# Kernel tuning notes

Hardware: AMD Instinct MI355X
Metric: run time of the kernel (lower is better)

## Reference

```python
import jax, jax.numpy as jnp
import numpy as np

B, N, IN_DIM = 2, 512, 512
MEM, HID = 300, 64
NEG_SLOPE = 0.01


def setup_inputs() -> dict:
    key = jax.random.key(0)
    ks = jax.random.split(key, 10)
    feature = jax.random.normal(ks[0], (B, N, IN_DIM), dtype=jnp.float32)
    adj = jax.random.randint(ks[1], (B, N, N), 0, 2).astype(jnp.float32)
    s = 0.05
    # per-layer node projections W[l]
    w0 = jax.random.normal(ks[2], (IN_DIM, MEM), dtype=jnp.float32) * s
    b0 = jnp.zeros((MEM,), dtype=jnp.float32)
    w1 = jax.random.normal(ks[3], (MEM, MEM), dtype=jnp.float32) * s
    b1 = jnp.zeros((MEM,), dtype=jnp.float32)
    # shared attention MLP (afcs): Linear(2*MEM, HID) -> ReLU -> Linear(HID, 1)
    a1_w = jax.random.normal(ks[4], (2 * MEM, HID), dtype=jnp.float32) * s
    a1_b = jnp.zeros((HID,), dtype=jnp.float32)
    a2_w = jax.random.normal(ks[5], (HID, 1), dtype=jnp.float32) * s
    a2_b = jnp.zeros((1,), dtype=jnp.float32)
    return {"feature": feature, "adj": adj, "w0": w0, "b0": b0, "w1": w1,
            "b1": b1, "a1_w": a1_w, "a1_b": a1_b, "a2_w": a2_w, "a2_b": a2_b}


def _gat_layer(h_in, adj, w, b, a1_w, a1_b, a2_w, a2_b):
    h = h_in @ w + b                                   # (B,N,M)
    # cat([h_i, h_j]) @ a1_w split into the two halves (same math, no N^2*2M tensor)
    s_i = h @ a1_w[:MEM]                               # (B,N,H)
    s_j = h @ a1_w[MEM:]                               # (B,N,H)
    z = jax.nn.relu(s_i[:, :, None, :] + s_j[:, None, :, :] + a1_b)   # (B,N,N,H)
    e = (z @ a2_w)[..., 0] + a2_b[0]                   # (B,N,N)
    e = jax.nn.leaky_relu(e, negative_slope=NEG_SLOPE)
    b_, n_ = adj.shape[0], adj.shape[1]
    dmask = adj.reshape(b_, n_ * n_)
    logits = e.reshape(b_, n_ * n_) * dmask + (1.0 - dmask) * (-1e30)
    # NOTE: softmax over ALL N*N flattened edges (faithful to original dim=1)
    att = jax.nn.softmax(logits, axis=1).reshape(b_, n_, n_)
    return jnp.einsum('bij,bjd->bid', att, h)


def reference(feature, adj, w0, b0, w1, b1, a1_w, a1_b, a2_w, a2_b):
    f = _gat_layer(feature, adj, w0, b0, a1_w, a1_b, a2_w, a2_b)
    f = _gat_layer(f, adj, w1, b1, a1_w, a1_b, a2_w, a2_b)  # dropout = identity (eval)
    return f
```

## Files before the change

### kernel.cpp

```cpp
#include <hip/hip_runtime.h>

namespace {

constexpr int B_  = 2;
constexpr int N_  = 512;
constexpr int IN_ = 512;
constexpr int M_  = 300;
constexpr int H_  = 64;
constexpr float SLOPE_ = 0.01f;

constexpr long OFF_CW1AI = 0;
constexpr long OFF_CW1AJ = OFF_CW1AI + 19200;
constexpr long OFF_BS1I  = OFF_CW1AJ + 19200;
constexpr long OFF_BS1J  = OFF_BS1I  + 64;
constexpr long OFF_H0S   = OFF_BS1J  + 64;
constexpr long OFF_SI0S  = OFF_H0S   + 3L * 307200;
constexpr long OFF_SJ0S  = OFF_SI0S  + 4L * 65536;
constexpr long OFF_F1S   = OFF_SJ0S  + 4L * 65536;
constexpr long OFF_H1S   = OFF_F1S   + 3L * 307200;
constexpr long OFF_SI1S  = OFF_H1S   + 2L * 307200;
constexpr long OFF_SJ1S  = OFF_SI1S  + 2L * 65536;
constexpr long OFF_ZP0   = OFF_SJ1S  + 2L * 65536;
constexpr long OFF_ZP1   = OFF_ZP0   + 512;
constexpr long OFF_P0    = OFF_ZP1   + 512;
constexpr long OFF_P1    = OFF_P0    + 524288;

__device__ __forceinline__ float4 f4add(float4 a, float4 b) {
    a.x += b.x; a.y += b.y; a.z += b.z; a.w += b.w; return a;
}

struct JobsK {
    const float* A[5]; long afs[5];
    const float* W[5]; long wfs[5];
    const float* bias[5]; const float* Zp[5];
    float* C[5]; long cslice[5];
    int K[5]; int lda[5]; int Cc[5]; int R[5]; int split[5];
    int off[5]; int njobs;
};

template<int TPB, int AFOLD, int WFOLD>
__global__ __launch_bounds__(TPB)
void gemm_jobs(JobsK jb)
{
    constexpr int TM  = (TPB == 256) ? 64 : 32;
    constexpr int TN  = TM;
    constexpr int APT = 32 * TM / TPB;
    constexpr int AQW = 32 / APT;
    constexpr int WQW = TPB / 32;
    constexpr int WPT = TN / WQW;
    constexpr int TCW = TN / 4;

    __shared__ __align__(16) float As[32][TM + 4];
    __shared__ __align__(16) float Ws[32][TN + 4];
    __shared__ float zred[4];

    const int bid = blockIdx.x;
    int j = jb.njobs - 1;
    while (j > 0 && bid < jb.off[j]) --j;
    const int local = bid - jb.off[j];

    const float* __restrict__ A = jb.A[j];  const long afs = jb.afs[j];
    const float* __restrict__ W = jb.W[j];  const long wfs = jb.wfs[j];
    const float* bias = jb.bias[j];
    const float* Zp   = jb.Zp[j];
    float* __restrict__ C = jb.C[j];
    const int K = jb.K[j], lda = jb.lda[j], Cc = jb.Cc[j], R = jb.R[j];
    const int split = jb.split[j];

    const int tx  = (Cc + TN - 1) / TN;
    const int ty  = (R + TM - 1) / TM;
    const int nrc = tx * ty;
    const int tile  = local % nrc;
    const int slice = local / nrc;
    const int row0 = (tile / tx) * TM;
    const int col0 = (tile % tx) * TN;
    const int nslab = (K + 31) >> 5;
    const int spl   = (nslab + split - 1) / split;
    const int kb    = slice * spl * 32;
    const int Ke    = min(K, kb + spl * 32);
    C += (long)slice * jb.cslice[j];

    const int t  = threadIdx.x;
    const int ar = t / AQW, aq = t % AQW;
    const int arow = min(row0 + ar, R - 1);
    const int wr = t / WQW, wq = t % WQW;
    const int tr = t / TCW, tc = t % TCW;

    float4 av[APT / 4], wv[WPT / 4];

    auto loadA = [&](int k0) {
        #pragma unroll
        for (int f = 0; f < APT / 4; ++f) {
            const int k = k0 + aq * APT + f * 4;
            const long base = (long)arow * lda + k;
            float4 r = make_float4(0.f, 0.f, 0.f, 0.f);
            if (k + 3 < Ke) {
                #pragma unroll
                for (int s = 0; s < AFOLD; ++s)
                    r = f4add(r, *(const float4*)(A + (long)s * afs + base));
            } else {
                #pragma unroll
                for (int u = 0; u < 4; ++u)
                    if (k + u < Ke) {
                        float v = 0.f;
                        #pragma unroll
                        for (int s = 0; s < AFOLD; ++s)
                            v += A[(long)s * afs + base + u];
                        (&r.x)[u] = v;
                    }
            }
            av[f] = r;
        }
    };
    auto loadW = [&](int k0) {
        const int gk = k0 + wr;
        #pragma unroll
        for (int f = 0; f < WPT / 4; ++f) {
            const int c = col0 + wq * WPT + f * 4;
            float4 r = make_float4(0.f, 0.f, 0.f, 0.f);
            if (gk < Ke) {
                const long base = (long)gk * Cc + c;
                if (c + 3 < Cc) {
                    #pragma unroll
                    for (int s = 0; s < WFOLD; ++s)
                        r = f4add(r, *(const float4*)(W + (long)s * wfs + base));
                } else {
                    #pragma unroll
                    for (int u = 0; u < 4; ++u)
                        if (c + u < Cc) {
                            float v = 0.f;
                            #pragma unroll
                            for (int s = 0; s < WFOLD; ++s)
                                v += W[(long)s * wfs + base + u];
                            (&r.x)[u] = v;
                        }
                }
            }
            wv[f] = r;
        }
    };

    float acc[4][4] = {};
    loadA(kb);
    loadW(kb);

    for (int k0 = kb; k0 < Ke; k0 += 32) {
        #pragma unroll
        for (int f = 0; f < APT / 4; ++f) {
            #pragma unroll
            for (int c = 0; c < 4; ++c) {
                const int kk = aq * APT + f * 4 + c;
                const int s  = (kk >> 3) & 3;
                As[kk][ar ^ (s << 2)] = (&av[f].x)[c];
            }
        }
        #pragma unroll
        for (int f = 0; f < WPT / 4; ++f)
            *(float4*)&Ws[wr][wq * WPT + 4 * f] = wv[f];
        __syncthreads();

        if (k0 + 32 < Ke) {
            loadA(k0 + 32);
            loadW(k0 + 32);
        }

        #pragma unroll
        for (int k = 0; k < 32; ++k) {
            const int s = (k >> 3) & 3;
            const float4 a4 = *(const float4*)&As[k][(tr ^ s) * 4];
            const float4 w4 = *(const float4*)&Ws[k][tc * 4];
            const float a_[4] = {a4.x, a4.y, a4.z, a4.w};
            #pragma unroll
            for (int i = 0; i < 4; ++i) {
                acc[i][0] = fmaf(a_[i], w4.x, acc[i][0]);
                acc[i][1] = fmaf(a_[i], w4.y, acc[i][1]);
                acc[i][2] = fmaf(a_[i], w4.z, acc[i][2]);
                acc[i][3] = fmaf(a_[i], w4.w, acc[i][3]);
            }
        }
        __syncthreads();
    }

    float scale = 1.0f;
    if (Zp != nullptr) {
        if constexpr (TPB == 256) {
            float v = Zp[t];
            #pragma unroll
            for (int off = 32; off > 0; off >>= 1)
                v += __shfl_down(v, off, 64);
            if ((t & 63) == 0) zred[t >> 6] = v;
            __syncthreads();
            scale = 1.0f / (zred[0] + zred[1] + zred[2] + zred[3]);
        } else {
            float v = Zp[t] + Zp[t + 64] + Zp[t + 128] + Zp[t + 192];
            #pragma unroll
            for (int off = 32; off > 0; off >>= 1)
                v += __shfl_down(v, off, 64);
            scale = 1.0f / __shfl(v, 0, 64);
        }
    }

    const int cbase = col0 + tc * 4;
    float bv[4] = {0.f, 0.f, 0.f, 0.f};
    if (bias != nullptr && slice == 0) {
        #pragma unroll
        for (int u = 0; u < 4; ++u)
            if (cbase + u < Cc) bv[u] = bias[cbase + u];
    }
    #pragma unroll
    for (int i = 0; i < 4; ++i) {
        const int r = row0 + tr * 4 + i;
        if (r < R) {
            if (cbase + 3 < Cc) {
                float4 o;
                o.x = fmaf(acc[i][0], scale, bv[0]);
                o.y = fmaf(acc[i][1], scale, bv[1]);
                o.z = fmaf(acc[i][2], scale, bv[2]);
                o.w = fmaf(acc[i][3], scale, bv[3]);
                *(float4*)(C + (long)r * Cc + cbase) = o;
            } else {
                #pragma unroll
                for (int u = 0; u < 4; ++u)
                    if (cbase + u < Cc)
                        C[(long)r * Cc + cbase + u] = fmaf(acc[i][u], scale, bv[u]);
            }
        }
    }
}

template<int FOLD>
__global__ __launch_bounds__(256)
void attn_k(const float* __restrict__ si, const float* __restrict__ sj,
            const float* __restrict__ adj, const float* __restrict__ a2w,
            const float* __restrict__ a2b, float* __restrict__ p,
            float* __restrict__ Zpart)
{
    __shared__ __align__(16) float Si[32][68];
    __shared__ __align__(16) float Sj[32][68];
    __shared__ float red[4];

    const int g    = blockIdx.x;
    const int b    = g >> 8;
    const int tile = g & 255;
    const int i0 = (tile >> 4) * 32;
    const int j0 = (tile & 15) * 32;
    const int t  = threadIdx.x;

    {
        const int r  = t >> 3;
        const int hc = (t & 7) * 8;
        const long gib = ((long)(b * N_ + i0 + r)) * H_ + hc;
        const long gjb = ((long)(b * N_ + j0 + r)) * H_ + hc;
        float4 a0 = make_float4(0.f, 0.f, 0.f, 0.f);
        float4 a1 = a0, b0v = a0, b1v = a0;
        #pragma unroll
        for (int s = 0; s < FOLD; ++s) {
            const float* gi = si + (long)s * 65536 + gib;
            const float* gj = sj + (long)s * 65536 + gjb;
            a0  = f4add(a0,  *(const float4*)(gi));
            a1  = f4add(a1,  *(const float4*)(gi + 4));
            b0v = f4add(b0v, *(const float4*)(gj));
            b1v = f4add(b1v, *(const float4*)(gj + 4));
        }
        *(float4*)&Si[r][hc]     = a0;
        *(float4*)&Si[r][hc + 4] = a1;
        *(float4*)&Sj[r][hc]     = b0v;
        *(float4*)&Sj[r][hc + 4] = b1v;
    }
    __syncthreads();

    const int i  = t >> 3;
    const int jl = t & 7;

    float e[4] = {0.f, 0.f, 0.f, 0.f};
    #pragma unroll
    for (int h0 = 0; h0 < H_; h0 += 4) {
        const float4 a4 = *(const float4*)&Si[i][h0];
        const float w0v = a2w[h0 + 0];
        const float w1v = a2w[h0 + 1];
        const float w2v = a2w[h0 + 2];
        const float w3v = a2w[h0 + 3];
        #pragma unroll
        for (int u = 0; u < 4; ++u) {
            const float4 b4 = *(const float4*)&Sj[jl + 8 * u][h0];
            e[u] = fmaf(fmaxf(a4.x + b4.x, 0.f), w0v, e[u]);
            e[u] = fmaf(fmaxf(a4.y + b4.y, 0.f), w1v, e[u]);
            e[u] = fmaf(fmaxf(a4.z + b4.z, 0.f), w2v, e[u]);
            e[u] = fmaf(fmaxf(a4.w + b4.w, 0.f), w3v, e[u]);
        }
    }

    const float a2bv = a2b[0];
    const long rowbase = ((long)(b * N_ + i0 + i)) * N_ + j0 + jl;
    float lsum = 0.f;
    #pragma unroll
    for (int u = 0; u < 4; ++u) {
        float ev = e[u] + a2bv;
        ev = (ev >= 0.f) ? ev : SLOPE_ * ev;
        const float m  = adj[rowbase + 8 * u];
        const float pv = m * __expf(ev);
        p[rowbase + 8 * u] = pv;
        lsum += pv;
    }

    #pragma unroll
    for (int off = 32; off > 0; off >>= 1)
        lsum += __shfl_down(lsum, off, 64);
    if ((t & 63) == 0) red[t >> 6] = lsum;
    __syncthreads();
    if (t == 0)
        Zpart[b * 256 + tile] = red[0] + red[1] + red[2] + red[3];
}

}

extern "C" void kernel_launch(void* const* d_in, const int* in_sizes, int n_in,
                              void* d_out, int out_size, void* d_ws, size_t ws_size,
                              hipStream_t stream)
{
    (void)in_sizes; (void)n_in; (void)out_size; (void)ws_size;
    const float* feature = (const float*)d_in[0];
    const float* adj     = (const float*)d_in[1];
    const float* w0      = (const float*)d_in[2];
    const float* b0      = (const float*)d_in[3];
    const float* w1      = (const float*)d_in[4];
    const float* b1      = (const float*)d_in[5];
    const float* a1w     = (const float*)d_in[6];
    const float* a1b     = (const float*)d_in[7];
    const float* a2w     = (const float*)d_in[8];
    const float* a2b     = (const float*)d_in[9];
    float* out = (float*)d_out;
    float* ws  = (float*)d_ws;

    float* cW1Ai = ws + OFF_CW1AI;
    float* cW1Aj = ws + OFF_CW1AJ;
    float* bs1i  = ws + OFF_BS1I;
    float* bs1j  = ws + OFF_BS1J;
    float* h0s   = ws + OFF_H0S;
    float* si0s  = ws + OFF_SI0S;
    float* sj0s  = ws + OFF_SJ0S;
    float* f1s   = ws + OFF_F1S;
    float* h1s   = ws + OFF_H1S;
    float* si1s  = ws + OFF_SI1S;
    float* sj1s  = ws + OFF_SJ1S;
    float* Zp0   = ws + OFF_ZP0;
    float* Zp1   = ws + OFF_ZP1;
    float* p0    = ws + OFF_P0;
    float* p1    = ws + OFF_P1;

    const float* Ai = a1w;
    const float* Aj = a1w + (long)M_ * H_;

    auto set_job = [](JobsK& jb, int j, const float* A, long afs,
                      const float* W, long wfs, const float* bias,
                      const float* Zp, float* C, long cslice,
                      int K, int lda, int Cc, int R, int split,
                      int TM, int& tiles) {
        jb.A[j] = A; jb.afs[j] = afs;
        jb.W[j] = W; jb.wfs[j] = wfs;
        jb.bias[j] = bias; jb.Zp[j] = Zp;
        jb.C[j] = C; jb.cslice[j] = cslice;
        jb.K[j] = K; jb.lda[j] = lda; jb.Cc[j] = Cc; jb.R[j] = R;
        jb.split[j] = split;
        jb.off[j] = tiles;
        tiles += ((R + TM - 1) / TM) * ((Cc + TM - 1) / TM) * split;
    };

    {
        JobsK jb; int tiles = 0;
        set_job(jb, 0, feature, 0, w0, 0, b0, nullptr, h0s, 307200,
                IN_, IN_, M_, 1024, 3, 64, tiles);
        set_job(jb, 1, w1, 0, Ai, 0, nullptr, nullptr, cW1Ai, 0,
                M_, M_, H_, M_, 1, 64, tiles);
        set_job(jb, 2, w1, 0, Aj, 0, nullptr, nullptr, cW1Aj, 0,
                M_, M_, H_, M_, 1, 64, tiles);
        set_job(jb, 3, b1, 0, Ai, 0, nullptr, nullptr, bs1i, 0,
                M_, M_, H_, 1, 1, 64, tiles);
        set_job(jb, 4, b1, 0, Aj, 0, a1b, nullptr, bs1j, 0,
                M_, M_, H_, 1, 1, 64, tiles);
        jb.njobs = 5;
        gemm_jobs<256, 1, 1><<<dim3(tiles), dim3(256), 0, stream>>>(jb);
    }

    {
        JobsK jb; int tiles = 0;
        set_job(jb, 0, h0s, 307200, Ai, 0, nullptr, nullptr, si0s, 65536,
                M_, M_, H_, 1024, 4, 64, tiles);
        set_job(jb, 1, h0s, 307200, Aj, 0, a1b, nullptr, sj0s, 65536,
                M_, M_, H_, 1024, 4, 64, tiles);
        jb.njobs = 2;
        gemm_jobs<256, 3, 1><<<dim3(tiles), dim3(256), 0, stream>>>(jb);
    }

    attn_k<4><<<dim3(512), dim3(256), 0, stream>>>(
        si0s, sj0s, adj, a2w, a2b, p0, Zp0);

    {
        JobsK jb; int tiles = 0;
        set_job(jb, 0, p0, 0, h0s, 307200, nullptr, Zp0, f1s, 307200,
                N_, N_, M_, N_, 3, 64, tiles);
        set_job(jb, 1, p0 + 262144, 0, h0s + 153600, 307200, nullptr,
                Zp0 + 256, f1s + 153600, 307200,
                N_, N_, M_, N_, 3, 64, tiles);
        jb.njobs = 2;
        gemm_jobs<256, 1, 3><<<dim3(tiles), dim3(256), 0, stream>>>(jb);
    }

    {
        JobsK jb; int tiles = 0;
        set_job(jb, 0, f1s, 307200, w1, 0, b1, nullptr, h1s, 307200,
                M_, M_, M_, 1024, 2, 64, tiles);
        set_job(jb, 1, f1s, 307200, cW1Ai, 0, bs1i, nullptr, si1s, 65536,
                M_, M_, H_, 1024, 2, 64, tiles);
        set_job(jb, 2, f1s, 307200, cW1Aj, 0, bs1j, nullptr, sj1s, 65536,
                M_, M_, H_, 1024, 2, 64, tiles);
        jb.njobs = 3;
        gemm_jobs<256, 3, 1><<<dim3(tiles), dim3(256), 0, stream>>>(jb);
    }

    attn_k<2><<<dim3(512), dim3(256), 0, stream>>>(
        si1s, sj1s, adj, a2w, a2b, p1, Zp1);

    {
        JobsK jb; int tiles = 0;
        set_job(jb, 0, p1, 0, h1s, 307200, nullptr, Zp1, out, 0,
                N_, N_, M_, N_, 1, 32, tiles);
        set_job(jb, 1, p1 + 262144, 0, h1s + 153600, 307200, nullptr,
                Zp1 + 256, out + 153600, 0,
                N_, N_, M_, N_, 1, 32, tiles);
        jb.njobs = 2;
        gemm_jobs<64, 1, 2><<<dim3(tiles), dim3(64), 0, stream>>>(jb);
    }
}
```

Measured before the change: 211.1 us.

## Fuse s_i/s_j projections into attention kernel and drop split-K partial buffers

Each attention block now computes its 32-row slices of s_i and s_j from h directly, so the separate s_i/s_j GEMM launches and their slice-sum buffers are gone. Split-K with partial-sum folding is removed from every GEMM, and the layer-1 h1 projection runs as extra blocks inside the second attention launch. This cuts the launch count from seven to five and removes intermediate global traffic. The cost is redundant projection work: every attention block recomputes s_i/s_j over K=300, roughly 16 times over, and the non-split GEMMs have fewer blocks, which lowers parallelism.

```diff
diff --git a/kernel.cpp b/kernel.cpp
--- a/kernel.cpp
+++ b/kernel.cpp
@@ -2,112 +2,55 @@
 
 namespace {
 
-constexpr int B_  = 2;
-constexpr int N_  = 512;
-constexpr int IN_ = 512;
-constexpr int M_  = 300;
-constexpr int H_  = 64;
+constexpr int N_ = 512;
+constexpr int M_ = 300;
+constexpr int H_ = 64;
 constexpr float SLOPE_ = 0.01f;
 
 constexpr long OFF_CW1AI = 0;
 constexpr long OFF_CW1AJ = OFF_CW1AI + 19200;
 constexpr long OFF_BS1I  = OFF_CW1AJ + 19200;
 constexpr long OFF_BS1J  = OFF_BS1I  + 64;
-constexpr long OFF_H0S   = OFF_BS1J  + 64;
-constexpr long OFF_SI0S  = OFF_H0S   + 3L * 307200;
-constexpr long OFF_SJ0S  = OFF_SI0S  + 4L * 65536;
-constexpr long OFF_F1S   = OFF_SJ0S  + 4L * 65536;
-constexpr long OFF_H1S   = OFF_F1S   + 3L * 307200;
-constexpr long OFF_SI1S  = OFF_H1S   + 2L * 307200;
-constexpr long OFF_SJ1S  = OFF_SI1S  + 2L * 65536;
-constexpr long OFF_ZP0   = OFF_SJ1S  + 2L * 65536;
+constexpr long OFF_H0    = OFF_BS1J  + 64;
+constexpr long OFF_F1    = OFF_H0    + 307200;
+constexpr long OFF_H1    = OFF_F1    + 307200;
+constexpr long OFF_ZP0   = OFF_H1    + 307200;
 constexpr long OFF_ZP1   = OFF_ZP0   + 512;
 constexpr long OFF_P0    = OFF_ZP1   + 512;
 constexpr long OFF_P1    = OFF_P0    + 524288;
 
-__device__ __forceinline__ float4 f4add(float4 a, float4 b) {
-    a.x += b.x; a.y += b.y; a.z += b.z; a.w += b.w; return a;
-}
-
-struct JobsK {
-    const float* A[5]; long afs[5];
-    const float* W[5]; long wfs[5];
-    const float* bias[5]; const float* Zp[5];
-    float* C[5]; long cslice[5];
-    int K[5]; int lda[5]; int Cc[5]; int R[5]; int split[5];
-    int off[5]; int njobs;
-};
-
-template<int TPB, int AFOLD, int WFOLD>
-__global__ __launch_bounds__(TPB)
-void gemm_jobs(JobsK jb)
+__device__ __forceinline__ void gemm_tile64(
+    const float* __restrict__ A, const float* __restrict__ W,
+    const float* __restrict__ bias, const float* __restrict__ Zp,
+    float* __restrict__ C, int K, int lda, int Cc, int R, int local,
+    float* smem)
 {
-    constexpr int TM  = (TPB == 256) ? 64 : 32;
-    constexpr int TN  = TM;
-    constexpr int APT = 32 * TM / TPB;
-    constexpr int AQW = 32 / APT;
-    constexpr int WQW = TPB / 32;
-    constexpr int WPT = TN / WQW;
-    constexpr int TCW = TN / 4;
-
-    __shared__ __align__(16) float As[32][TM + 4];
-    __shared__ __align__(16) float Ws[32][TN + 4];
-    __shared__ float zred[4];
-
-    const int bid = blockIdx.x;
-    int j = jb.njobs - 1;
-    while (j > 0 && bid < jb.off[j]) --j;
-    const int local = bid - jb.off[j];
-
-    const float* __restrict__ A = jb.A[j];  const long afs = jb.afs[j];
-    const float* __restrict__ W = jb.W[j];  const long wfs = jb.wfs[j];
-    const float* bias = jb.bias[j];
-    const float* Zp   = jb.Zp[j];
-    float* __restrict__ C = jb.C[j];
-    const int K = jb.K[j], lda = jb.lda[j], Cc = jb.Cc[j], R = jb.R[j];
-    const int split = jb.split[j];
-
-    const int tx  = (Cc + TN - 1) / TN;
-    const int ty  = (R + TM - 1) / TM;
-    const int nrc = tx * ty;
-    const int tile  = local % nrc;
-    const int slice = local / nrc;
-    const int row0 = (tile / tx) * TM;
-    const int col0 = (tile % tx) * TN;
-    const int nslab = (K + 31) >> 5;
-    const int spl   = (nslab + split - 1) / split;
-    const int kb    = slice * spl * 32;
-    const int Ke    = min(K, kb + spl * 32);
-    C += (long)slice * jb.cslice[j];
+    float (*As)[68] = (float(*)[68])smem;
+    float (*Ws)[68] = (float(*)[68])(smem + 2176);
+    float* zred = smem + 4352;
+
+    const int tx   = (Cc + 63) >> 6;
+    const int row0 = (local / tx) * 64;
+    const int col0 = (local % tx) * 64;
 
     const int t  = threadIdx.x;
-    const int ar = t / AQW, aq = t % AQW;
+    const int ar = t >> 2, aq = t & 3;
     const int arow = min(row0 + ar, R - 1);
-    const int wr = t / WQW, wq = t % WQW;
-    const int tr = t / TCW, tc = t % TCW;
-
-    float4 av[APT / 4], wv[WPT / 4];
-
+    const int wr = t >> 3, wq = t & 7;
+    const int tr = t >> 4, tc = t & 15;
+
+    float4 av[2], wv[2];
     auto loadA = [&](int k0) {
         #pragma unroll
-        for (int f = 0; f < APT / 4; ++f) {
-            const int k = k0 + aq * APT + f * 4;
-            const long base = (long)arow * lda + k;
+        for (int f = 0; f < 2; ++f) {
+            const int k = k0 + aq * 8 + f * 4;
             float4 r = make_float4(0.f, 0.f, 0.f, 0.f);
-            if (k + 3 < Ke) {
-                #pragma unroll
-                for (int s = 0; s < AFOLD; ++s)
-                    r = f4add(r, *(const float4*)(A + (long)s * afs + base));
+            if (k + 3 < K) {
+                r = *(const float4*)(A + (long)arow * lda + k);
             } else {
                 #pragma unroll
                 for (int u = 0; u < 4; ++u)
-                    if (k + u < Ke) {
-                        float v = 0.f;
-                        #pragma unroll
-                        for (int s = 0; s < AFOLD; ++s)
-                            v += A[(long)s * afs + base + u];
-                        (&r.x)[u] = v;
-                    }
+                    if (k + u < K) (&r.x)[u] = A[(long)arow * lda + k + u];
             }
             av[f] = r;
         }
@@ -115,25 +58,16 @@
     auto loadW = [&](int k0) {
         const int gk = k0 + wr;
         #pragma unroll
-        for (int f = 0; f < WPT / 4; ++f) {
-            const int c = col0 + wq * WPT + f * 4;
+        for (int f = 0; f < 2; ++f) {
+            const int c = col0 + wq * 8 + f * 4;
             float4 r = make_float4(0.f, 0.f, 0.f, 0.f);
-            if (gk < Ke) {
-                const long base = (long)gk * Cc + c;
+            if (gk < K) {
                 if (c + 3 < Cc) {
-                    #pragma unroll
-                    for (int s = 0; s < WFOLD; ++s)
-                        r = f4add(r, *(const float4*)(W + (long)s * wfs + base));
+                    r = *(const float4*)(W + (long)gk * Cc + c);
                 } else {
                     #pragma unroll
                     for (int u = 0; u < 4; ++u)
-                        if (c + u < Cc) {
-                            float v = 0.f;
-                            #pragma unroll
-                            for (int s = 0; s < WFOLD; ++s)
-                                v += W[(long)s * wfs + base + u];
-                            (&r.x)[u] = v;
-                        }
+                        if (c + u < Cc) (&r.x)[u] = W[(long)gk * Cc + c + u];
                 }
             }
             wv[f] = r;
@@ -141,28 +75,24 @@
     };
 
     float acc[4][4] = {};
-    loadA(kb);
-    loadW(kb);
-
-    for (int k0 = kb; k0 < Ke; k0 += 32) {
-        #pragma unroll
-        for (int f = 0; f < APT / 4; ++f) {
+    loadA(0);
+    loadW(0);
+
+    for (int k0 = 0; k0 < K; k0 += 32) {
+        #pragma unroll
+        for (int f = 0; f < 2; ++f)
             #pragma unroll
             for (int c = 0; c < 4; ++c) {
-                const int kk = aq * APT + f * 4 + c;
+                const int kk = aq * 8 + f * 4 + c;
                 const int s  = (kk >> 3) & 3;
                 As[kk][ar ^ (s << 2)] = (&av[f].x)[c];
             }
-        }
-        #pragma unroll
-        for (int f = 0; f < WPT / 4; ++f)
-            *(float4*)&Ws[wr][wq * WPT + 4 * f] = wv[f];
+        #pragma unroll
+        for (int f = 0; f < 2; ++f)
+            *(float4*)&Ws[wr][wq * 8 + 4 * f] = wv[f];
         __syncthreads();
 
-        if (k0 + 32 < Ke) {
-            loadA(k0 + 32);
-            loadW(k0 + 32);
-        }
+        if (k0 + 32 < K) { loadA(k0 + 32); loadW(k0 + 32); }
 
         #pragma unroll
         for (int k = 0; k < 32; ++k) {
@@ -183,26 +113,18 @@
 
     float scale = 1.0f;
     if (Zp != nullptr) {
-        if constexpr (TPB == 256) {
-            float v = Zp[t];
-            #pragma unroll
-            for (int off = 32; off > 0; off >>= 1)
-                v += __shfl_down(v, off, 64);
-            if ((t & 63) == 0) zred[t >> 6] = v;
-            __syncthreads();
-            scale = 1.0f / (zred[0] + zred[1] + zred[2] + zred[3]);
-        } else {
-            float v = Zp[t] + Zp[t + 64] + Zp[t + 128] + Zp[t + 192];
-            #pragma unroll
-            for (int off = 32; off > 0; off >>= 1)
-                v += __shfl_down(v, off, 64);
-            scale = 1.0f / __shfl(v, 0, 64);
-        }
+        float v = Zp[t];
+        #pragma unroll
+        for (int off = 32; off > 0; off >>= 1)
+            v += __shfl_down(v, off, 64);
+        if ((t & 63) == 0) zred[t >> 6] = v;
+        __syncthreads();
+        scale = 1.0f / (zred[0] + zred[1] + zred[2] + zred[3]);
     }
 
     const int cbase = col0 + tc * 4;
     float bv[4] = {0.f, 0.f, 0.f, 0.f};
-    if (bias != nullptr && slice == 0) {
+    if (bias != nullptr) {
         #pragma unroll
         for (int u = 0; u < 4; ++u)
             if (cbase + u < Cc) bv[u] = bias[cbase + u];
@@ -228,45 +150,135 @@
     }
 }
 
-template<int FOLD>
+struct JobsK {
+    const float* A[5]; const float* W[5]; const float* bias[5];
+    const float* Zp[5]; float* C[5];
+    int K[5]; int lda[5]; int Cc[5]; int R[5];
+    int off[5]; int njobs;
+};
+
 __global__ __launch_bounds__(256)
-void attn_k(const float* __restrict__ si, const float* __restrict__ sj,
-            const float* __restrict__ adj, const float* __restrict__ a2w,
-            const float* __restrict__ a2b, float* __restrict__ p,
-            float* __restrict__ Zpart)
+void gemm_jobs(JobsK jb)
 {
-    __shared__ __align__(16) float Si[32][68];
-    __shared__ __align__(16) float Sj[32][68];
+    __shared__ __align__(16) float smem[4360];
+    const int bid = blockIdx.x;
+    int j = jb.njobs - 1;
+    while (j > 0 && bid < jb.off[j]) --j;
+    gemm_tile64(jb.A[j], jb.W[j], jb.bias[j], jb.Zp[j], jb.C[j],
+                jb.K[j], jb.lda[j], jb.Cc[j], jb.R[j], bid - jb.off[j], smem);
+}
+
+__global__ __launch_bounds__(256)
+void attn_plus(const float* __restrict__ h, const float* __restrict__ Wi,
+               const float* __restrict__ Wj, const float* __restrict__ bi,
+               const float* __restrict__ bj, const float* __restrict__ adj,
+               const float* __restrict__ a2w, const float* __restrict__ a2b,
+               float* __restrict__ p, float* __restrict__ Zpart,
+               const float* gA, const float* gW, const float* gbias,
+               float* gC, int gK, int glda, int gCc, int gR)
+{
+    __shared__ __align__(16) float smem[6656];
     __shared__ float red[4];
 
-    const int g    = blockIdx.x;
-    const int b    = g >> 8;
-    const int tile = g & 255;
+    const int bid = blockIdx.x;
+    if (bid >= 512) {
+        gemm_tile64(gA, gW, gbias, nullptr, gC, gK, glda, gCc, gR,
+                    bid - 512, smem);
+        return;
+    }
+
+    float* Hi  = smem;
+    float* Hj  = smem + 1152;
+    float* WAi = smem + 2304;
+    float* WAj = smem + 4480;
+
+    const int b    = bid >> 8;
+    const int tile = bid & 255;
     const int i0 = (tile >> 4) * 32;
     const int j0 = (tile & 15) * 32;
     const int t  = threadIdx.x;
 
-    {
-        const int r  = t >> 3;
-        const int hc = (t & 7) * 8;
-        const long gib = ((long)(b * N_ + i0 + r)) * H_ + hc;
-        const long gjb = ((long)(b * N_ + j0 + r)) * H_ + hc;
-        float4 a0 = make_float4(0.f, 0.f, 0.f, 0.f);
-        float4 a1 = a0, b0v = a0, b1v = a0;
-        #pragma unroll
-        for (int s = 0; s < FOLD; ++s) {
-            const float* gi = si + (long)s * 65536 + gib;
-            const float* gj = sj + (long)s * 65536 + gjb;
-            a0  = f4add(a0,  *(const float4*)(gi));
-            a1  = f4add(a1,  *(const float4*)(gi + 4));
-            b0v = f4add(b0v, *(const float4*)(gj));
-            b1v = f4add(b1v, *(const float4*)(gj + 4));
-        }
-        *(float4*)&Si[r][hc]     = a0;
-        *(float4*)&Si[r][hc + 4] = a1;
-        *(float4*)&Sj[r][hc]     = b0v;
-        *(float4*)&Sj[r][hc + 4] = b1v;
-    }
+    const int tm0 = (t >> 4) * 2;
+    const int tn0 = (t & 15) * 4;
+    const int hr  = t >> 3;
+    const int hk  = (t & 7) * 4;
+    const int wc0 = (t & 7) * 8;
+
+    float acci[2][4] = {}, accj[2][4] = {};
+
+    for (int k0 = 0; k0 < M_; k0 += 32) {
+        {
+            const int k = k0 + hk;
+            float4 hi4 = make_float4(0.f, 0.f, 0.f, 0.f), hj4 = hi4;
+            if (k + 3 < M_) {
+                hi4 = *(const float4*)(h + ((long)(b * N_ + i0 + hr)) * M_ + k);
+                hj4 = *(const float4*)(h + ((long)(b * N_ + j0 + hr)) * M_ + k);
+            }
+            *(float4*)&Hi[hr * 36 + hk] = hi4;
+            *(float4*)&Hj[hr * 36 + hk] = hj4;
+
+            const int wrow = k0 + hr;
+            float4 wi0 = make_float4(0.f, 0.f, 0.f, 0.f);
+            float4 wi1 = wi0, wj0 = wi0, wj1 = wi0;
+            if (wrow < M_) {
+                wi0 = *(const float4*)(Wi + (long)wrow * H_ + wc0);
+                wi1 = *(const float4*)(Wi + (long)wrow * H_ + wc0 + 4);
+                wj0 = *(const float4*)(Wj + (long)wrow * H_ + wc0);
+                wj1 = *(const float4*)(Wj + (long)wrow * H_ + wc0 + 4);
+            }
+            *(float4*)&WAi[hr * 68 + wc0]     = wi0;
+            *(float4*)&WAi[hr * 68 + wc0 + 4] = wi1;
+            *(float4*)&WAj[hr * 68 + wc0]     = wj0;
+            *(float4*)&WAj[hr * 68 + wc0 + 4] = wj1;
+        }
+        __syncthreads();
+
+        #pragma unroll
+        for (int k = 0; k < 32; ++k) {
+            const float ai0 = Hi[tm0 * 36 + k];
+            const float ai1 = Hi[(tm0 + 1) * 36 + k];
+            const float aj0 = Hj[tm0 * 36 + k];
+            const float aj1 = Hj[(tm0 + 1) * 36 + k];
+            const float4 wi = *(const float4*)&WAi[k * 68 + tn0];
+            const float4 wj = *(const float4*)&WAj[k * 68 + tn0];
+            acci[0][0] = fmaf(ai0, wi.x, acci[0][0]);
+            acci[0][1] = fmaf(ai0, wi.y, acci[0][1]);
+            acci[0][2] = fmaf(ai0, wi.z, acci[0][2]);
+            acci[0][3] = fmaf(ai0, wi.w, acci[0][3]);
+            acci[1][0] = fmaf(ai1, wi.x, acci[1][0]);
+            acci[1][1] = fmaf(ai1, wi.y, acci[1][1]);
+            acci[1][2] = fmaf(ai1, wi.z, acci[1][2]);
+            acci[1][3] = fmaf(ai1, wi.w, acci[1][3]);
+            accj[0][0] = fmaf(aj0, wj.x, accj[0][0]);
+            accj[0][1] = fmaf(aj0, wj.y, accj[0][1]);
+            accj[0][2] = fmaf(aj0, wj.z, accj[0][2]);
+            accj[0][3] = fmaf(aj0, wj.w, accj[0][3]);
+            accj[1][0] = fmaf(aj1, wj.x, accj[1][0]);
+            accj[1][1] = fmaf(aj1, wj.y, accj[1][1]);
+            accj[1][2] = fmaf(aj1, wj.z, accj[1][2]);
+            accj[1][3] = fmaf(aj1, wj.w, accj[1][3]);
+        }
+        __syncthreads();
+    }
+
+    float biv[4] = {0.f, 0.f, 0.f, 0.f};
+    float bjv[4];
+    if (bi != nullptr) {
+        #pragma unroll
+        for (int u = 0; u < 4; ++u) biv[u] = bi[tn0 + u];
+    }
+    #pragma unroll
+    for (int u = 0; u < 4; ++u) bjv[u] = bj[tn0 + u];
+
+    float* Si = smem;
+    float* Sj = smem + 2176;
+    #pragma unroll
+    for (int ii = 0; ii < 2; ++ii)
+        #pragma unroll
+        for (int u = 0; u < 4; ++u) {
+            Si[(tm0 + ii) * 68 + tn0 + u] = acci[ii][u] + biv[u];
+            Sj[(tm0 + ii) * 68 + tn0 + u] = accj[ii][u] + bjv[u];
+        }
     __syncthreads();
 
     const int i  = t >> 3;
@@ -274,15 +286,15 @@
 
     float e[4] = {0.f, 0.f, 0.f, 0.f};
     #pragma unroll
-    for (int h0 = 0; h0 < H_; h0 += 4) {
-        const float4 a4 = *(const float4*)&Si[i][h0];
-        const float w0v = a2w[h0 + 0];
-        const float w1v = a2w[h0 + 1];
-        const float w2v = a2w[h0 + 2];
-        const float w3v = a2w[h0 + 3];
+    for (int hh = 0; hh < H_; hh += 4) {
+        const float4 a4 = *(const float4*)&Si[i * 68 + hh];
+        const float w0v = a2w[hh + 0];
+        const float w1v = a2w[hh + 1];
+        const float w2v = a2w[hh + 2];
+        const float w3v = a2w[hh + 3];
         #pragma unroll
         for (int u = 0; u < 4; ++u) {
-            const float4 b4 = *(const float4*)&Sj[jl + 8 * u][h0];
+            const float4 b4 = *(const float4*)&Sj[(jl + 8 * u) * 68 + hh];
             e[u] = fmaf(fmaxf(a4.x + b4.x, 0.f), w0v, e[u]);
             e[u] = fmaf(fmaxf(a4.y + b4.y, 0.f), w1v, e[u]);
             e[u] = fmaf(fmaxf(a4.z + b4.z, 0.f), w2v, e[u]);
@@ -336,13 +348,9 @@
     float* cW1Aj = ws + OFF_CW1AJ;
     float* bs1i  = ws + OFF_BS1I;
     float* bs1j  = ws + OFF_BS1J;
-    float* h0s   = ws + OFF_H0S;
-    float* si0s  = ws + OFF_SI0S;
-    float* sj0s  = ws + OFF_SJ0S;
-    float* f1s   = ws + OFF_F1S;
-    float* h1s   = ws + OFF_H1S;
-    float* si1s  = ws + OFF_SI1S;
-    float* sj1s  = ws + OFF_SJ1S;
+    float* h0    = ws + OFF_H0;
+    float* f1    = ws + OFF_F1;
+    float* h1    = ws + OFF_H1;
     float* Zp0   = ws + OFF_ZP0;
     float* Zp1   = ws + OFF_ZP1;
     float* p0    = ws + OFF_P0;
@@ -351,84 +359,51 @@
     const float* Ai = a1w;
     const float* Aj = a1w + (long)M_ * H_;
 
-    auto set_job = [](JobsK& jb, int j, const float* A, long afs,
-                      const float* W, long wfs, const float* bias,
-                      const float* Zp, float* C, long cslice,
-                      int K, int lda, int Cc, int R, int split,
-                      int TM, int& tiles) {
-        jb.A[j] = A; jb.afs[j] = afs;
-        jb.W[j] = W; jb.wfs[j] = wfs;
-        jb.bias[j] = bias; jb.Zp[j] = Zp;
-        jb.C[j] = C; jb.cslice[j] = cslice;
+    auto set_job = [](JobsK& jb, int j, const float* A, const float* W,
+                      const float* bias, const float* Zp, float* C,
+                      int K, int lda, int Cc, int R, int& tiles) {
+        jb.A[j] = A; jb.W[j] = W; jb.bias[j] = bias; jb.Zp[j] = Zp; jb.C[j] = C;
         jb.K[j] = K; jb.lda[j] = lda; jb.Cc[j] = Cc; jb.R[j] = R;
-        jb.split[j] = split;
         jb.off[j] = tiles;
-        tiles += ((R + TM - 1) / TM) * ((Cc + TM - 1) / TM) * split;
+        tiles += ((R + 63) / 64) * ((Cc + 63) / 64);
     };
 
     {
         JobsK jb; int tiles = 0;
-        set_job(jb, 0, feature, 0, w0, 0, b0, nullptr, h0s, 307200,
-                IN_, IN_, M_, 1024, 3, 64, tiles);
-        set_job(jb, 1, w1, 0, Ai, 0, nullptr, nullptr, cW1Ai, 0,
-                M_, M_, H_, M_, 1, 64, tiles);
-        set_job(jb, 2, w1, 0, Aj, 0, nullptr, nullptr, cW1Aj, 0,
-                M_, M_, H_, M_, 1, 64, tiles);
-        set_job(jb, 3, b1, 0, Ai, 0, nullptr, nullptr, bs1i, 0,
-                M_, M_, H_, 1, 1, 64, tiles);
-        set_job(jb, 4, b1, 0, Aj, 0, a1b, nullptr, bs1j, 0,
-                M_, M_, H_, 1, 1, 64, tiles);
+        set_job(jb, 0, feature, w0, b0,   nullptr, h0,    512, 512, M_, 1024, tiles);
+        set_job(jb, 1, w1, Ai, nullptr, nullptr, cW1Ai, M_, M_, H_, M_, tiles);
+        set_job(jb, 2, w1, Aj, nullptr, nullptr, cW1Aj, M_, M_, H_, M_, tiles);
+        set_job(jb, 3, b1, Ai, nullptr, nullptr, bs1i,  M_, M_, H_, 1,  tiles);
+        set_job(jb, 4, b1, Aj, a1b,     nullptr, bs1j,  M_, M_, H_, 1,  tiles);
         jb.njobs = 5;
-        gemm_jobs<256, 1, 1><<<dim3(tiles), dim3(256), 0, stream>>>(jb);
-    }
+        gemm_jobs<<<dim3(tiles), dim3(256), 0, stream>>>(jb);
+    }
+
+    attn_plus<<<dim3(512), dim3(256), 0, stream>>>(
+        h0, Ai, Aj, nullptr, a1b, adj, a2w, a2b, p0, Zp0,
+        nullptr, nullptr, nullptr, nullptr, 0, 0, 0, 0);
 
     {
         JobsK jb; int tiles = 0;
-        set_job(jb, 0, h0s, 307200, Ai, 0, nullptr, nullptr, si0s, 65536,
-                M_, M_, H_, 1024, 4, 64, tiles);
-        set_job(jb, 1, h0s, 307200, Aj, 0, a1b, nullptr, sj0s, 65536,
-                M_, M_, H_, 1024, 4, 64, tiles);
+        set_job(jb, 0, p0,          h0,              nullptr, Zp0,       f1,
+                512, 512, M_, 512, tiles);
+        set_job(jb, 1, p0 + 262144, h0 + (long)N_*M_, nullptr, Zp0 + 256,
+                f1 + (long)N_*M_, 512, 512, M_, 512, tiles);
         jb.njobs = 2;
-        gemm_jobs<256, 3, 1><<<dim3(tiles), dim3(256), 0, stream>>>(jb);
-    }
-
-    attn_k<4><<<dim3(512), dim3(256), 0, stream>>>(
-        si0s, sj0s, adj, a2w, a2b, p0, Zp0);
+        gemm_jobs<<<dim3(tiles), dim3(256), 0, stream>>>(jb);
+    }
+
+    attn_plus<<<dim3(512 + 80), dim3(256), 0, stream>>>(
+        f1, cW1Ai, cW1Aj, bs1i, bs1j, adj, a2w, a2b, p1, Zp1,
+        f1, w1, b1, h1, M_, M_, M_, 1024);
 
     {
         JobsK jb; int tiles = 0;
-        set_job(jb, 0, p0, 0, h0s, 307200, nullptr, Zp0, f1s, 307200,
-                N_, N_, M_, N_, 3, 64, tiles);
-        set_job(jb, 1, p0 + 262144, 0, h0s + 153600, 307200, nullptr,
-                Zp0 + 256, f1s + 153600, 307200,
-                N_, N_, M_, N_, 3, 64, tiles);
+        set_job(jb, 0, p1,          h1,              nullptr, Zp1,       out,
+                512, 512, M_, 512, tiles);
+        set_job(jb, 1, p1 + 262144, h1 + (long)N_*M_, nullptr, Zp1 + 256,
+                out + (long)N_*M_, 512, 512, M_, 512, tiles);
         jb.njobs = 2;
-        gemm_jobs<256, 1, 3><<<dim3(tiles), dim3(256), 0, stream>>>(jb);
-    }
-
-    {
-        JobsK jb; int tiles = 0;
-        set_job(jb, 0, f1s, 307200, w1, 0, b1, nullptr, h1s, 307200,
-                M_, M_, M_, 1024, 2, 64, tiles);
-        set_job(jb, 1, f1s, 307200, cW1Ai, 0, bs1i, nullptr, si1s, 65536,
-                M_, M_, H_, 1024, 2, 64, tiles);
-        set_job(jb, 2, f1s, 307200, cW1Aj, 0, bs1j, nullptr, sj1s, 65536,
-                M_, M_, H_, 1024, 2, 64, tiles);
-        jb.njobs = 3;
-        gemm_jobs<256, 3, 1><<<dim3(tiles), dim3(256), 0, stream>>>(jb);
-    }
-
-    attn_k<2><<<dim3(512), dim3(256), 0, stream>>>(
-        si1s, sj1s, adj, a2w, a2b, p1, Zp1);
-
-    {
-        JobsK jb; int tiles = 0;
-        set_job(jb, 0, p1, 0, h1s, 307200, nullptr, Zp1, out, 0,
-                N_, N_, M_, N_, 1, 32, tiles);
-        set_job(jb, 1, p1 + 262144, 0, h1s + 153600, 307200, nullptr,
-                Zp1 + 256, out + 153600, 0,
-                N_, N_, M_, N_, 1, 32, tiles);
-        jb.njobs = 2;
-        gemm_jobs<64, 1, 2><<<dim3(tiles), dim3(64), 0, stream>>>(jb);
+        gemm_jobs<<<dim3(tiles), dim3(256), 0, stream>>>(jb);
     }
 }
```

Result: slower. 216.5 us (+2.6%).
